# Kernel tuning notes

Measured on AMD Instinct MI355X. Metric: run time of the kernel, lower is better.

Reference implementation:

```python
import jax, jax.numpy as jnp
import numpy as np

# module config (matches init_kwargs)
H, W, C = 32, 32, 3
KH, KW, KC = 4, 4, 1
N_CLASS = 10
NBIN = 200
SHIFT = (0, 0)
NH, NW, NC = H // KH, W // KW, C // KC
NKERNEL = NH * NW * NC          # 192
NDIM_SUB = KH * KW * KC         # 16
NCOMP = NDIM_SUB                # n_component defaults to ndim_sub
NDIM = H * W * C                # 3072
NTRANS = NKERNEL * NCOMP        # 3072
N = 2048


def setup_inputs() -> dict:
    key = jax.random.key(0)
    k1, k2, k3, k4, k5, k6 = jax.random.split(key, 6)
    data = jax.random.normal(k1, (N, NDIM), dtype=jnp.float32)
    label = jax.random.randint(k2, (N,), 0, N_CLASS)
    # per-patch orthonormal projections: QR with sign fix, as in __init__
    wi = jax.random.normal(k3, (NKERNEL, NDIM_SUB, NCOMP), dtype=jnp.float32)
    Q, R = jnp.linalg.qr(wi)
    sign = jnp.sign(jnp.diagonal(R, axis1=-2, axis2=-1))
    wT_blocks = Q * sign[:, None, :]
    # monotone rational-quadratic spline knots per class / transformed dim
    dx = jax.random.uniform(k4, (N_CLASS, NTRANS, NBIN - 1), minval=0.5, maxval=1.5)
    dy = jax.random.uniform(k5, (N_CLASS, NTRANS, NBIN - 1), minval=0.5, maxval=1.5)
    z = jnp.zeros((N_CLASS, NTRANS, 1), jnp.float32)
    knots_x = -4.0 + 8.0 * jnp.concatenate([z, jnp.cumsum(dx, -1)], -1) / jnp.sum(dx, -1, keepdims=True)
    knots_y = -4.0 + 8.0 * jnp.concatenate([z, jnp.cumsum(dy, -1)], -1) / jnp.sum(dy, -1, keepdims=True)
    knots_d = jax.random.uniform(k6, (N_CLASS, NTRANS, NBIN), minval=0.5, maxval=1.5)
    return {"data": data, "label": label, "wT_blocks": wT_blocks,
            "knots_x": knots_x.astype(jnp.float32), "knots_y": knots_y.astype(jnp.float32),
            "knots_d": knots_d}


def construct_wT(wT_blocks):
    """Assemble block-structured (NDIM, NTRANS) projection from per-patch blocks."""
    dim = jnp.arange(NDIM).reshape(H, W, C)
    dim = jnp.roll(dim, (-SHIFT[0], -SHIFT[1]), axis=(0, 1))  # Shift() == negative roll
    # rows[b] = flat pixel indices of patch b; block order index = h*NW*NC + w*NC + c
    rows = dim.reshape(NH, KH, NW, KW, C).transpose(0, 2, 4, 1, 3).reshape(NKERNEL, NDIM_SUB)
    cols = jnp.arange(NKERNEL)[:, None] * NCOMP + jnp.arange(NCOMP)[None, :]
    wT = jnp.zeros((NDIM, NTRANS), wT_blocks.dtype)
    return wT.at[rows[:, :, None], cols[:, None, :]].set(wT_blocks)


def rq_spline(x, xx, yy, dd):
    """Monotone rational-quadratic spline with linear extrapolation.
    x: (N, T); xx/yy/dd: (T, K) knot positions / values / derivatives.
    Returns (y, log|dy/dx|), each (N, T)."""
    xT = x.T  # (T, N)
    lo, hi = xx[:, :1], xx[:, -1:]
    below, above = xT < lo, xT > hi
    xc = jnp.clip(xT, lo, hi)  # keep interior branch NaN-free
    k = jax.vmap(lambda kn, v: jnp.searchsorted(kn, v, side='right'))(xx, xc) - 1
    k = jnp.clip(k, 0, NBIN - 2)
    take = lambda a, i: jnp.take_along_axis(a, i, axis=1)
    xk, xk1 = take(xx, k), take(xx, k + 1)
    yk, yk1 = take(yy, k), take(yy, k + 1)
    dk, dk1 = take(dd, k), take(dd, k + 1)
    wdt = xk1 - xk
    s = (yk1 - yk) / wdt
    xi = (xc - xk) / wdt
    om = 1.0 - xi
    denom = s + (dk1 + dk - 2.0 * s) * xi * om
    ys = yk + (yk1 - yk) * (s * xi * xi + dk * xi * om) / denom
    lj_s = 2.0 * jnp.log(s) + jnp.log(dk1 * xi * xi + 2.0 * s * xi * om + dk * om * om) - 2.0 * jnp.log(denom)
    d0, dK = dd[:, :1], dd[:, -1:]
    y = jnp.where(below, yy[:, :1] + (xT - lo) * d0,
                  jnp.where(above, yy[:, -1:] + (xT - hi) * dK, ys))
    lj = jnp.where(below, jnp.log(d0), jnp.where(above, jnp.log(dK), lj_s))
    return y.T, lj.T


def reference(data, label, wT_blocks, knots_x, knots_y, knots_d):
    wT = construct_wT(wT_blocks)                 # (NDIM, NTRANS)
    data0 = data @ wT                            # (N, NTRANS)
    remaining = data - data0 @ wT.T              # orthogonal complement (zero here since full-rank)

    def body(carry, params):
        c, data1, logj = carry
        xx, yy, dd = params
        y, lj = rq_spline(data0, xx, yy, dd)
        m = label == c
        data1 = jnp.where(m[:, None], y, data1)
        logj = jnp.where(m, jnp.sum(lj, axis=1), logj)
        return (c + 1, data1, logj), None

    init = (jnp.int32(0), jnp.zeros_like(data0), jnp.zeros((data.shape[0],), data.dtype))
    (_, data1, logj), _ = jax.lax.scan(body, init, (knots_x, knots_y, knots_d))
    out = remaining + data1 @ wT.T
    return out, logj
```

## Files before the change

### kernel.cpp

```cpp
#include <hip/hip_runtime.h>

constexpr int NSAMP  = 2048;
constexpr int NDIM   = 3072;
constexpr int NTRANS = 3072;
constexpr int NBIN   = 200;
constexpr int NCLASS = 10;
constexpr int NPATCH = 192;
constexpr int BLK    = 256;
constexpr int PER_T  = NDIM / BLK;
constexpr int DSTR   = 20;
constexpr int SA     = 4;
constexpr int SC     = 4;
constexpr int NL     = 128;
constexpr int LUTS   = 136;

__device__ __forceinline__ float4* xb_line(float* xb, int p, int sl) {
    return (float4*)(xb + ((size_t)p * NSAMP + (sl ^ (p & 63))) * 16);
}
__device__ __forceinline__ const float4* xb_line_c(const float* xb, int p, int sl) {
    return (const float4*)(xb + ((size_t)p * NSAMP + (sl ^ (p & 63))) * 16);
}

__global__ __launch_bounds__(1024)
void p0_prep(const int* __restrict__ label,
             const float* __restrict__ B,
             int* __restrict__ slot,
             int* __restrict__ cls_off,
             float* __restrict__ Bt)
{
    __shared__ int s_lab[NSAMP];
    __shared__ int s_cnt[32][NCLASS];
    __shared__ int s_pre[32][NCLASS];
    __shared__ int s_tot[NCLASS];
    __shared__ int s_off[NCLASS + 1];
    const int tid  = threadIdx.x;
    const int lane = tid & 63;
    const int wv   = tid >> 6;

    for (int i = tid; i < NSAMP; i += 1024) s_lab[i] = label[i];
    for (int e = tid; e < NPATCH * 256; e += 1024) {
        const int p = e >> 8, r = e & 255;
        Bt[p * 256 + (r & 15) * 16 + (r >> 4)] = B[e];
    }
    __syncthreads();

    const unsigned long long ltmask = ((unsigned long long)1 << lane) - 1;
    int myrank[2], myc[2];
    #pragma unroll
    for (int pass = 0; pass < 2; ++pass) {
        const int n = pass * 1024 + tid;
        const int c = s_lab[n];
        myc[pass] = c;
        int r = 0;
        #pragma unroll
        for (int cls = 0; cls < NCLASS; ++cls) {
            const unsigned long long b = __ballot(c == cls);
            if (lane == 0) s_cnt[pass * 16 + wv][cls] = __popcll(b);
            if (cls == c)  r = __popcll(b & ltmask);
        }
        myrank[pass] = r;
    }
    __syncthreads();

    if (tid < 32 * NCLASS) {
        const int seg = tid & 31;
        const int cls = tid >> 5;
        int acc = 0;
        for (int s = 0; s < seg; ++s) acc += s_cnt[s][cls];
        s_pre[seg][cls] = acc;
        if (seg == 31) s_tot[cls] = acc + s_cnt[31][cls];
    }
    __syncthreads();
    if (tid == 0) {
        int a = 0;
        for (int c = 0; c < NCLASS; ++c) { s_off[c] = a; a += s_tot[c]; }
        s_off[NCLASS] = a;
    }
    __syncthreads();

    #pragma unroll
    for (int pass = 0; pass < 2; ++pass) {
        const int n   = pass * 1024 + tid;
        const int seg = pass * 16 + wv;
        const int c   = myc[pass];
        slot[n] = s_off[c] + s_pre[seg][c] + myrank[pass];
    }
    if (tid <= NCLASS) cls_off[tid] = s_off[tid];
}

__global__ __launch_bounds__(BLK, 4)
void pA_project(const float* __restrict__ data,
                const float* __restrict__ Bt,
                const int*   __restrict__ slot,
                float* __restrict__ xb)
{
    __shared__ float s_data[SA][NDIM];
    const int b   = blockIdx.x;
    const int tid = threadIdx.x;
    const int n0  = b * SA;

    #pragma unroll
    for (int s = 0; s < SA; ++s) {
        const float4* dr = (const float4*)(data + (size_t)(n0 + s) * NDIM);
        float4* sd = (float4*)s_data[s];
        #pragma unroll
        for (int j = 0; j < 3; ++j)
            sd[tid + BLK * j] = dr[tid + BLK * j];
    }
    int sls[SA];
    #pragma unroll
    for (int s = 0; s < SA; ++s) sls[s] = slot[n0 + s];
    __syncthreads();

    #pragma unroll 1
    for (int jj = 0; jj < 3; ++jj) {
        const int tau = tid + BLK * jj;
        const int p   = tau >> 2;
        const int q4  = tau & 3;
        const int nh  = p / 24;
        const int rem = p - nh * 24;
        const int nw  = rem / 3;
        const int ch  = rem - nw * 3;
        const int rowbase = nh * 384 + nw * 12 + ch;

        float4 Bp[16];
        const float4* Bg = (const float4*)(Bt + p * 256 + q4 * 64);
        #pragma unroll
        for (int i = 0; i < 16; ++i) Bp[i] = Bg[i];

        #pragma unroll
        for (int s = 0; s < SA; ++s) {
            float dv[16];
            #pragma unroll
            for (int i = 0; i < 16; ++i)
                dv[i] = s_data[s][rowbase + (i >> 2) * 96 + (i & 3) * 3];

            float acc[4];
            #pragma unroll
            for (int cc = 0; cc < 4; ++cc) {
                float a = 0.f;
                #pragma unroll
                for (int q = 0; q < 4; ++q) {
                    const float4 bv = Bp[cc * 4 + q];
                    a += bv.x * dv[q * 4 + 0] + bv.y * dv[q * 4 + 1]
                       + bv.z * dv[q * 4 + 2] + bv.w * dv[q * 4 + 3];
                }
                acc[cc] = a;
            }
            *(xb_line(xb, p, sls[s]) + q4) =
                make_float4(acc[0], acc[1], acc[2], acc[3]);
        }
    }
}

__global__ __launch_bounds__(BLK, 8)
void pB_spline(const float* __restrict__ kx,
               const float* __restrict__ ky,
               const float* __restrict__ kd,
               const int*   __restrict__ cls_off,
               float* __restrict__ xb,
               float* __restrict__ ljpart)
{
    __shared__ float s_kx[16 * NBIN];
    __shared__ unsigned char s_lut[16 * LUTS];

    const int p   = blockIdx.x;
    const int c   = blockIdx.y;
    const int tid = threadIdx.x;
    const int t0  = p * 16;

    const size_t kofs = ((size_t)c * NTRANS + t0) * NBIN;
    const float4* gx = (const float4*)(kx + kofs);
    float4* lx = (float4*)s_kx;
    #pragma unroll 1
    for (int i = tid; i < 16 * NBIN / 4; i += BLK) lx[i] = gx[i];
    __syncthreads();

    {
        const int r  = tid >> 4;
        const int ch = tid & 15;
        const float* xx = s_kx + r * NBIN;
        const int j0 = ch * 8;
        const float xu0 = -4.0f + (float)j0 * (8.0f / NL);
        int klo = 0, khi = NBIN;
        #pragma unroll
        for (int it = 0; it < 8; ++it) {
            const int mid = (klo + khi) >> 1;
            const bool le = (xx[mid] <= xu0);
            klo = le ? mid : klo;
            khi = le ? khi : mid;
        }
        int k = klo;
        const int nj = (ch == 15) ? 9 : 8;
        unsigned char* lrow = s_lut + r * LUTS + j0;
        #pragma unroll 1
        for (int jj = 0; jj < nj; ++jj) {
            const float xuj = -4.0f + (float)(j0 + jj) * (8.0f / NL);
            while (k < NBIN - 1 && xx[k + 1] <= xuj) ++k;
            lrow[jj] = (unsigned char)k;
        }
    }
    __syncthreads();

    const int qq  = tid & 3;
    const int sid = tid >> 2;
    const float* sxx = s_kx + qq * 4 * NBIN;
    const float* kyp = ky + kofs + (size_t)(qq * 4) * NBIN;
    const float* kdp = kd + kofs + (size_t)(qq * 4) * NBIN;

    const int beg = cls_off[c];
    const int end = cls_off[c + 1];

    for (int s0 = beg; s0 < end; s0 += 64) {
        const int sl = s0 + sid;
        if (sl < end) {
            float4* line = xb_line(xb, p, sl) + qq;
            const float4 v = *line;
            float xs[4] = {v.x, v.y, v.z, v.w};

            float lj_sum = 0.f;
            #pragma unroll
            for (int j = 0; j < 4; ++j) {
                const float* xx  = sxx + j * NBIN;
                const float* yyg = kyp + j * NBIN;
                const float* ddg = kdp + j * NBIN;
                const unsigned char* lrow = s_lut + (qq * 4 + j) * LUTS;
                const float x  = xs[j];
                const float lo = xx[0];
                const float hi = xx[NBIN - 1];

                float y, lj;
                if (x < lo) {
                    const float d0 = ddg[0];
                    y  = yyg[0] + (x - lo) * d0;
                    lj = __logf(d0);
                } else if (x > hi) {
                    const float dK = ddg[NBIN - 1];
                    y  = yyg[NBIN - 1] + (x - hi) * dK;
                    lj = __logf(dK);
                } else {
                    int u = (int)((x + 4.0f) * (NL / 8.0f));
                    u = u < 0 ? 0 : (u > NL - 1 ? NL - 1 : u);
                    int klo = (int)lrow[u] - 1;
                    klo = klo < 0 ? 0 : klo;
                    int khi = (int)lrow[u + 1] + 2;
                    khi = khi > NBIN ? NBIN : khi;
                    #pragma unroll
                    for (int it = 0; it < 3; ++it) {
                        const int mid = (klo + khi) >> 1;
                        const bool le = (xx[mid] <= x);
                        klo = le ? mid : klo;
                        khi = le ? khi : mid;
                    }
                    int k = klo;
                    if (k > NBIN - 2) k = NBIN - 2;

                    const float xk = xx[k], xk1 = xx[k + 1];
                    const float yk = yyg[k], yk1 = yyg[k + 1];
                    const float dk = ddg[k], dk1 = ddg[k + 1];

                    const float wdt     = xk1 - xk;
                    const float inv_wdt = __fdividef(1.f, wdt);
                    const float dy      = yk1 - yk;
                    const float s       = dy * inv_wdt;
                    const float xi      = (x - xk) * inv_wdt;
                    const float om      = 1.f - xi;
                    const float denom   = s + (dk1 + dk - 2.f * s) * xi * om;
                    const float r       = __fdividef(1.f, denom);
                    const float num     = dy * (s * xi * xi + dk * xi * om);
                    y = yk + num * r;
                    const float Nq = dk1 * xi * xi + 2.f * s * xi * om + dk * om * om;
                    const float t2 = s * r;
                    lj = __logf(t2 * t2 * Nq);
                }
                xs[j] = y - x;
                lj_sum += lj;
            }

            *line = make_float4(xs[0], xs[1], xs[2], xs[3]);

            lj_sum += __shfl_xor(lj_sum, 1);
            lj_sum += __shfl_xor(lj_sum, 2);
            if (qq == 0) ljpart[(size_t)p * NSAMP + sl] = lj_sum;
        }
    }
}

__global__ __launch_bounds__(BLK)
void p_ljred(const float* __restrict__ ljpart,
             float* __restrict__ logj_slot)
{
    const int sl = blockIdx.x * BLK + threadIdx.x;
    float a0 = 0.f, a1 = 0.f, a2 = 0.f, a3 = 0.f;
    #pragma unroll 1
    for (int g = 0; g < NPATCH; g += 4) {
        a0 += ljpart[(size_t)(g + 0) * NSAMP + sl];
        a1 += ljpart[(size_t)(g + 1) * NSAMP + sl];
        a2 += ljpart[(size_t)(g + 2) * NSAMP + sl];
        a3 += ljpart[(size_t)(g + 3) * NSAMP + sl];
    }
    logj_slot[sl] = (a0 + a1) + (a2 + a3);
}

__global__ __launch_bounds__(BLK, 2)
void pC_recon(const float* __restrict__ data,
              const float* __restrict__ B,
              const int*   __restrict__ slot,
              const float* __restrict__ xb,
              const float* __restrict__ logj_slot,
              float* __restrict__ out,
              float* __restrict__ logj)
{
    __shared__ float s_diff[SC][NPATCH * DSTR];
    const int b   = blockIdx.x;
    const int tid = threadIdx.x;
    const int n0  = b * SC;

    #pragma unroll
    for (int s = 0; s < SC; ++s) {
        const int sl = slot[n0 + s];
        #pragma unroll
        for (int jj = 0; jj < 3; ++jj) {
            const int i  = tid + BLK * jj;
            const int pp = i >> 2;
            const int q  = i & 3;
            const float4 v = *(xb_line_c(xb, pp, sl) + q);
            *(float4*)&s_diff[s][pp * DSTR + q * 4] = v;
        }
    }
    if (tid < SC) logj[n0 + tid] = logj_slot[slot[n0 + tid]];
    __syncthreads();

    #pragma unroll 1
    for (int j = 0; j < PER_T; ++j) {
        const int d  = tid + BLK * j;
        const int ch = d % 3;
        const int hw = d / 3;
        const int w  = hw & 31;
        const int h  = hw >> 5;
        const int p  = ((h >> 2) * 8 + (w >> 2)) * 3 + ch;
        const int i  = (h & 3) * 4 + (w & 3);

        const float4* Bp4 = (const float4*)(B + p * 256 + i * 16);
        const float4 b0 = Bp4[0], b1 = Bp4[1], b2 = Bp4[2], b3 = Bp4[3];

        #pragma unroll
        for (int s = 0; s < SC; ++s) {
            const float4* dp4 = (const float4*)&s_diff[s][p * DSTR];
            const float4 d0 = dp4[0], d1 = dp4[1], d2 = dp4[2], d3 = dp4[3];
            float acc = data[(size_t)(n0 + s) * NDIM + d];
            acc += b0.x * d0.x + b0.y * d0.y + b0.z * d0.z + b0.w * d0.w;
            acc += b1.x * d1.x + b1.y * d1.y + b1.z * d1.z + b1.w * d1.w;
            acc += b2.x * d2.x + b2.y * d2.y + b2.z * d2.z + b2.w * d2.w;
            acc += b3.x * d3.x + b3.y * d3.y + b3.z * d3.z + b3.w * d3.w;
            out[(size_t)(n0 + s) * NDIM + d] = acc;
        }
    }
}

extern "C" void kernel_launch(void* const* d_in, const int* in_sizes, int n_in,
                              void* d_out, int out_size, void* d_ws, size_t ws_size,
                              hipStream_t stream) {
    const float* data  = (const float*)d_in[0];
    const int*   label = (const int*)  d_in[1];
    const float* B     = (const float*)d_in[2];
    const float* kx    = (const float*)d_in[3];
    const float* ky    = (const float*)d_in[4];
    const float* kd    = (const float*)d_in[5];

    float* out  = (float*)d_out;
    float* logj = (float*)d_out + (size_t)NSAMP * NDIM;

    char* ws = (char*)d_ws;
    size_t off = 0;
    float* xb        = (float*)(ws + off); off += (size_t)NPATCH * NSAMP * 16 * 4;
    float* ljpart    = (float*)(ws + off); off += (size_t)NPATCH * NSAMP * 4;
    float* Bt        = (float*)(ws + off); off += (size_t)NPATCH * 256 * 4;
    float* logj_slot = (float*)(ws + off); off += NSAMP * 4;
    int*   slot      = (int*)  (ws + off); off += NSAMP * 4;
    int*   cls_off   = (int*)  (ws + off); off += 64;

    p0_prep   <<<1, 1024, 0, stream>>>(label, B, slot, cls_off, Bt);
    pA_project<<<NSAMP / SA, BLK, 0, stream>>>(data, Bt, slot, xb);
    dim3 gridB(NPATCH, NCLASS);
    pB_spline <<<gridB, BLK, 0, stream>>>(kx, ky, kd, cls_off, xb, ljpart);
    p_ljred   <<<NSAMP / BLK, BLK, 0, stream>>>(ljpart, logj_slot);
    pC_recon  <<<NSAMP / SC, BLK, 0, stream>>>(data, B, slot, xb, logj_slot, out, logj);
}
```

Baseline: 239.8 us.

## Drop B transpose and logj reduction kernel; atomically accumulate logj, prefetch spline loads

```diff
diff --git a/kernel.cpp b/kernel.cpp
--- a/kernel.cpp
+++ b/kernel.cpp
@@ -23,10 +23,9 @@
 
 __global__ __launch_bounds__(1024)
 void p0_prep(const int* __restrict__ label,
-             const float* __restrict__ B,
              int* __restrict__ slot,
              int* __restrict__ cls_off,
-             float* __restrict__ Bt)
+             float* __restrict__ logj_slot)
 {
     __shared__ int s_lab[NSAMP];
     __shared__ int s_cnt[32][NCLASS];
@@ -37,10 +36,9 @@
     const int lane = tid & 63;
     const int wv   = tid >> 6;
 
-    for (int i = tid; i < NSAMP; i += 1024) s_lab[i] = label[i];
-    for (int e = tid; e < NPATCH * 256; e += 1024) {
-        const int p = e >> 8, r = e & 255;
-        Bt[p * 256 + (r & 15) * 16 + (r >> 4)] = B[e];
+    for (int i = tid; i < NSAMP; i += 1024) {
+        s_lab[i] = label[i];
+        logj_slot[i] = 0.f;
     }
     __syncthreads();
 
@@ -90,7 +88,7 @@
 
 __global__ __launch_bounds__(BLK, 4)
 void pA_project(const float* __restrict__ data,
-                const float* __restrict__ Bt,
+                const float* __restrict__ B,
                 const int*   __restrict__ slot,
                 float* __restrict__ xb)
 {
@@ -124,9 +122,9 @@
         const int rowbase = nh * 384 + nw * 12 + ch;
 
         float4 Bp[16];
-        const float4* Bg = (const float4*)(Bt + p * 256 + q4 * 64);
-        #pragma unroll
-        for (int i = 0; i < 16; ++i) Bp[i] = Bg[i];
+        const float4* Bg = (const float4*)(B + p * 256 + q4 * 4);
+        #pragma unroll
+        for (int i = 0; i < 16; ++i) Bp[i] = Bg[i * 4];
 
         #pragma unroll
         for (int s = 0; s < SA; ++s) {
@@ -135,17 +133,13 @@
             for (int i = 0; i < 16; ++i)
                 dv[i] = s_data[s][rowbase + (i >> 2) * 96 + (i & 3) * 3];
 
-            float acc[4];
+            float acc[4] = {0.f, 0.f, 0.f, 0.f};
             #pragma unroll
-            for (int cc = 0; cc < 4; ++cc) {
-                float a = 0.f;
-                #pragma unroll
-                for (int q = 0; q < 4; ++q) {
-                    const float4 bv = Bp[cc * 4 + q];
-                    a += bv.x * dv[q * 4 + 0] + bv.y * dv[q * 4 + 1]
-                       + bv.z * dv[q * 4 + 2] + bv.w * dv[q * 4 + 3];
-                }
-                acc[cc] = a;
+            for (int i = 0; i < 16; ++i) {
+                acc[0] += Bp[i].x * dv[i];
+                acc[1] += Bp[i].y * dv[i];
+                acc[2] += Bp[i].z * dv[i];
+                acc[3] += Bp[i].w * dv[i];
             }
             *(xb_line(xb, p, sls[s]) + q4) =
                 make_float4(acc[0], acc[1], acc[2], acc[3]);
@@ -159,7 +153,7 @@
                const float* __restrict__ kd,
                const int*   __restrict__ cls_off,
                float* __restrict__ xb,
-               float* __restrict__ ljpart)
+               float* __restrict__ logj_slot)
 {
     __shared__ float s_kx[16 * NBIN];
     __shared__ unsigned char s_lut[16 * LUTS];
@@ -210,14 +204,22 @@
 
     const int beg = cls_off[c];
     const int end = cls_off[c + 1];
-
-    for (int s0 = beg; s0 < end; s0 += 64) {
-        const int sl = s0 + sid;
-        if (sl < end) {
-            float4* line = xb_line(xb, p, sl) + qq;
-            const float4 v = *line;
+    const int nit = (end - beg + 63) >> 6;
+
+    int sl = beg + sid;
+    float4 v = make_float4(0.f, 0.f, 0.f, 0.f);
+    float4* lcur = nullptr;
+    if (sl < end) { lcur = xb_line(xb, p, sl) + qq; v = *lcur; }
+
+    #pragma unroll 1
+    for (int it = 0; it < nit; ++it) {
+        const int sln = sl + 64;
+        float4 vn = make_float4(0.f, 0.f, 0.f, 0.f);
+        float4* lnx = nullptr;
+        if (it + 1 < nit && sln < end) { lnx = xb_line(xb, p, sln) + qq; vn = *lnx; }
+
+        if (lcur) {
             float xs[4] = {v.x, v.y, v.z, v.w};
-
             float lj_sum = 0.f;
             #pragma unroll
             for (int j = 0; j < 4; ++j) {
@@ -246,7 +248,7 @@
                     int khi = (int)lrow[u + 1] + 2;
                     khi = khi > NBIN ? NBIN : khi;
                     #pragma unroll
-                    for (int it = 0; it < 3; ++it) {
+                    for (int itb = 0; itb < 3; ++itb) {
                         const int mid = (klo + khi) >> 1;
                         const bool le = (xx[mid] <= x);
                         klo = le ? mid : klo;
@@ -277,29 +279,15 @@
                 lj_sum += lj;
             }
 
-            *line = make_float4(xs[0], xs[1], xs[2], xs[3]);
+            *lcur = make_float4(xs[0], xs[1], xs[2], xs[3]);
 
             lj_sum += __shfl_xor(lj_sum, 1);
             lj_sum += __shfl_xor(lj_sum, 2);
-            if (qq == 0) ljpart[(size_t)p * NSAMP + sl] = lj_sum;
-        }
-    }
-}
-
-__global__ __launch_bounds__(BLK)
-void p_ljred(const float* __restrict__ ljpart,
-             float* __restrict__ logj_slot)
-{
-    const int sl = blockIdx.x * BLK + threadIdx.x;
-    float a0 = 0.f, a1 = 0.f, a2 = 0.f, a3 = 0.f;
-    #pragma unroll 1
-    for (int g = 0; g < NPATCH; g += 4) {
-        a0 += ljpart[(size_t)(g + 0) * NSAMP + sl];
-        a1 += ljpart[(size_t)(g + 1) * NSAMP + sl];
-        a2 += ljpart[(size_t)(g + 2) * NSAMP + sl];
-        a3 += ljpart[(size_t)(g + 3) * NSAMP + sl];
-    }
-    logj_slot[sl] = (a0 + a1) + (a2 + a3);
+            if (qq == 0) atomicAdd(&logj_slot[sl], lj_sum);
+        }
+
+        sl = sln; lcur = lnx; v = vn;
+    }
 }
 
 __global__ __launch_bounds__(BLK, 2)
@@ -374,16 +362,13 @@
     char* ws = (char*)d_ws;
     size_t off = 0;
     float* xb        = (float*)(ws + off); off += (size_t)NPATCH * NSAMP * 16 * 4;
-    float* ljpart    = (float*)(ws + off); off += (size_t)NPATCH * NSAMP * 4;
-    float* Bt        = (float*)(ws + off); off += (size_t)NPATCH * 256 * 4;
     float* logj_slot = (float*)(ws + off); off += NSAMP * 4;
     int*   slot      = (int*)  (ws + off); off += NSAMP * 4;
     int*   cls_off   = (int*)  (ws + off); off += 64;
 
-    p0_prep   <<<1, 1024, 0, stream>>>(label, B, slot, cls_off, Bt);
-    pA_project<<<NSAMP / SA, BLK, 0, stream>>>(data, Bt, slot, xb);
+    p0_prep   <<<1, 1024, 0, stream>>>(label, slot, cls_off, logj_slot);
+    pA_project<<<NSAMP / SA, BLK, 0, stream>>>(data, B, slot, xb);
     dim3 gridB(NPATCH, NCLASS);
-    pB_spline <<<gridB, BLK, 0, stream>>>(kx, ky, kd, cls_off, xb, ljpart);
-    p_ljred   <<<NSAMP / BLK, BLK, 0, stream>>>(ljpart, logj_slot);
+    pB_spline <<<gridB, BLK, 0, stream>>>(kx, ky, kd, cls_off, xb, logj_slot);
     pC_recon  <<<NSAMP / SC, BLK, 0, stream>>>(data, B, slot, xb, logj_slot, out, logj);
 }
```

Measured after the change: 199.8 us. 16.7% less time.
